# Performance work log

Hardware: AMD Instinct MI355X
Metric: run time of the kernel (lower is better)

## Reference

```python
import jax, jax.numpy as jnp
import numpy as np
from jax import lax

N, H, W = 8, 512, 512
INF = 1.0e6  # sentinel distance; INF**2 = 1e12 fits fp32


def _edt(feature):
    """Exact Euclidean distance transform. feature: (N,H,W) bool, True = zero-distance pixels.
    Separable: 1D column-distance per row via two scans, then min over rows of (di^2 + g^2).
    (cv2 DIST_L2 mask=3 is a chamfer approximation of this exact EDT.)"""
    g = jnp.where(feature, 0.0, INF)  # (N,H,W)
    cols = jnp.moveaxis(g, 2, 0)  # (W,N,H)

    def step(c, x):
        d = jnp.minimum(x, c + 1.0)
        return d, d

    init = jnp.full(g.shape[:2], INF, g.dtype)
    _, f = lax.scan(step, init, cols)
    _, b = lax.scan(step, init, f, reverse=True)
    g1 = jnp.moveaxis(b, 0, 2)  # (N,H,W) 1D distance along W
    g2 = g1 * g1
    rows = jnp.arange(g.shape[1], dtype=g.dtype)

    def per_row(i):
        # min over source rows k of (i-k)^2 + g2[:,k,:] -> (N,W)
        return jnp.min(g2 + ((i - rows) ** 2)[None, :, None], axis=1)

    d2 = lax.map(per_row, rows)  # (H,N,W)
    return jnp.sqrt(jnp.moveaxis(d2, 0, 1))  # (N,H,W)


def _signed_distance(gt):
    # gt: (N,1,H,W). Positive inside mask, negative outside; per-image normalized, clipped to [-1,1].
    m = gt[:, 0] > 0.5
    dist_in = _edt(~m)   # cv2.distanceTransform(m): distance to nearest zero pixel
    dist_out = _edt(m)   # cv2.distanceTransform(1-m)
    sd = dist_in - dist_out
    mx = jnp.max(sd, axis=(1, 2), keepdims=True)
    sd = jnp.where(mx > 0, sd / (mx + 1e-6), sd)
    return jnp.clip(sd, -1.0, 1.0)[:, None]  # (N,1,H,W)


def _bce(p, t):
    eps = 1e-7  # stand-in for torch BCELoss log clamp at -100
    p = jnp.clip(p, eps, 1.0 - eps)
    return -(t * jnp.log(p) + (1.0 - t) * jnp.log1p(-p))


def _loss(seg_pred, seg_gt, edge_pred, edge_gt,
          cb_edge=0.9, lam_dice=0.5, w_edge=0.5, w_boundary=0.2):
    # seg = BCE + lam_dice * Dice
    seg_bce = jnp.mean(_bce(seg_pred, seg_gt))
    inter = jnp.sum(seg_pred * seg_gt, axis=(2, 3))
    denom = jnp.sum(seg_pred, axis=(2, 3)) + jnp.sum(seg_gt, axis=(2, 3)) + 1e-6
    dice = 1.0 - jnp.mean(2.0 * inter / denom)
    seg = seg_bce + lam_dice * dice
    # edge = class-balanced BCE
    el = _bce(edge_pred, edge_gt)
    w = jnp.where(edge_gt > 0.5, cb_edge, 1.0 - cb_edge)
    edg = jnp.mean(el * w) * w_edge
    # boundary = |pred-gt| * |signed distance of gt| (sd is detached in the original)
    sd = lax.stop_gradient(_signed_distance(seg_gt))
    bdl = w_boundary * jnp.mean(jnp.abs(seg_pred - seg_gt) * jnp.abs(sd))
    return seg + edg + bdl


def setup_inputs() -> dict:
    key = jax.random.key(0)
    k1, k2, k3, k4 = jax.random.split(key, 4)
    shp = (N, 1, H, W)
    return {
        "seg_pred": jax.random.uniform(k1, shp, dtype=jnp.float32),
        "seg_gt": (jax.random.uniform(k2, shp) > 0.5).astype(jnp.float32),
        "edge_pred": jax.random.uniform(k3, shp, dtype=jnp.float32),
        "edge_gt": (jax.random.uniform(k4, shp) > 0.5).astype(jnp.float32),
    }


def reference(seg_pred, seg_gt, edge_pred, edge_gt):
    return _loss(seg_pred, seg_gt, edge_pred, edge_gt)
```

## Files before the change

### kernel.cpp

```cpp
#include <hip/hip_runtime.h>
#include <math.h>

#define HN 8
#define HH 512
#define HW 512
#define NPIX (HH*HW)
#define NTOT (HN*NPIX)
#define INF1D 1.0e6f
#define BIGF 3.0e38f
#define SQINF 4.4e9f

__global__ __launch_bounds__(256) void k_rows(const float* __restrict__ gt,
                                              unsigned int* __restrict__ packed) {
  const int lane = threadIdx.x & 63;
  const int wv   = threadIdx.x >> 6;
  const int row  = blockIdx.x * 4 + wv;
  const float* g = gt + (size_t)row * HW;

  float4 a0 = *(const float4*)(g + lane * 8);
  float4 a1 = *(const float4*)(g + lane * 8 + 4);
  float mv[8] = {a0.x, a0.y, a0.z, a0.w, a1.x, a1.y, a1.z, a1.w};

  float pin[8], pout[8], sfin[8], sfout[8];
  float rin = BIGF, rout = BIGF;
  for (int j = 0; j < 8; ++j) {
    float wf = (float)(lane * 8 + j);
    bool m = mv[j] > 0.5f;
    float gin  = m ? INF1D : 0.f;
    float gout = m ? 0.f : INF1D;
    rin  = fminf(rin,  gin  - wf);  pin[j]  = rin;
    rout = fminf(rout, gout - wf);  pout[j] = rout;
  }
  float xin = rin, xout = rout;
  for (int off = 1; off < 64; off <<= 1) {
    float yi = __shfl_up(xin, off);
    float yo = __shfl_up(xout, off);
    if (lane >= off) { xin = fminf(xin, yi); xout = fminf(xout, yo); }
  }
  float ein  = __shfl_up(xin, 1);  if (lane == 0) ein  = BIGF;
  float eout = __shfl_up(xout, 1); if (lane == 0) eout = BIGF;

  float rsin = BIGF, rsout = BIGF;
  for (int j = 7; j >= 0; --j) {
    float wf = (float)(lane * 8 + j);
    bool m = mv[j] > 0.5f;
    float gin  = m ? INF1D : 0.f;
    float gout = m ? 0.f : INF1D;
    rsin  = fminf(rsin,  gin  + wf);  sfin[j]  = rsin;
    rsout = fminf(rsout, gout + wf);  sfout[j] = rsout;
  }
  float zin = rsin, zout = rsout;
  for (int off = 1; off < 64; off <<= 1) {
    float yi = __shfl_down(zin, off);
    float yo = __shfl_down(zout, off);
    if (lane + off < 64) { zin = fminf(zin, yi); zout = fminf(zout, yo); }
  }
  float sein  = __shfl_down(zin, 1);  if (lane == 63) sein  = BIGF;
  float seout = __shfl_down(zout, 1); if (lane == 63) seout = BIGF;

  unsigned int outp[8];
  for (int j = 0; j < 8; ++j) {
    float wf = (float)(lane * 8 + j);
    float fin  = wf + fminf(pin[j],  ein);
    float fout = wf + fminf(pout[j], eout);
    float bin  = fminf(sfin[j],  sein)  - wf;
    float bout = fminf(sfout[j], seout) - wf;
    float g1i = fminf(fin,  bin);
    float g1o = fminf(fout, bout);
    unsigned int di = (g1i > 65534.f) ? 0xFFFFu : (unsigned int)(g1i + 0.5f);
    unsigned int dq = (g1o > 65534.f) ? 0xFFFFu : (unsigned int)(g1o + 0.5f);
    outp[j] = di | (dq << 16);
  }
  unsigned int* dst = packed + (size_t)row * HW + lane * 8;
  *(uint4*)dst       = make_uint4(outp[0], outp[1], outp[2], outp[3]);
  *(uint4*)(dst + 4) = make_uint4(outp[4], outp[5], outp[6], outp[7]);
}

#define ICH 64
#define HALO 32
__global__ __launch_bounds__(256) void k_cols(const unsigned int* __restrict__ packed,
                                              float* __restrict__ sd,
                                              float* __restrict__ partials) {
  __shared__ float sq[128 * 65];
  const int tid = threadIdx.x;
  const int wx = blockIdx.x;
  const int iy = blockIdx.y;
  const int n  = blockIdx.z;
  const int I0 = iy * ICH;
  const int kb = max(0, I0 - HALO);
  const int ke = min(HH, I0 + ICH + HALO);
  const int sz = ke - kb;
  const int w0 = wx * 64;
  const unsigned int* src = packed + (size_t)n * NPIX + (size_t)kb * HW + w0;

  const int total4 = sz * 16;
  for (int p4 = tid; p4 < total4; p4 += 256) {
    int row = p4 >> 4;
    int c4  = (p4 & 15) << 2;
    uint4 v = *(const uint4*)(src + (size_t)row * HW + c4);
    unsigned int u[4] = {v.x, v.y, v.z, v.w};
#pragma unroll
    for (int e = 0; e < 4; ++e) {
      unsigned int lo = u[e] & 0xFFFFu;
      unsigned int hi = u[e] >> 16;
      unsigned int d  = lo | hi;
      float dsq = (float)(d * d);
      sq[row * 65 + c4 + e] = (hi == 0u) ? dsq : -dsq;
    }
  }
  __syncthreads();

  const int lane = tid & 63;
  const int wv   = tid >> 6;
  const int col  = lane;
  const int base = (I0 - kb) + wv * 16;
  float lmax = -BIGF;

  for (int q = 0; q < 16; ++q) {
    const int li = base + q;
    const float own = sq[li * 65 + col];
    const bool  m   = own > 0.f;
    const float sgn = m ? 1.f : -1.f;
    float best = fabsf(own);
#pragma unroll
    for (int dk = 1; dk <= 8; ++dk) {
      const float dkk = (float)(dk * dk);
      int k1 = li - dk, k2 = li + dk;
      float a = sgn * sq[max(k1, 0) * 65 + col];
      float b = sgn * sq[min(k2, sz - 1) * 65 + col];
      float ta = (k1 >= 0) ? fmaxf(a, 0.f) : SQINF;
      float tb = (k2 < sz) ? fmaxf(b, 0.f) : SQINF;
      best = fminf(best, ta + dkk);
      best = fminf(best, tb + dkk);
    }
    for (int dk = 9; dk < 128; ++dk) {
      float dkk = (float)(dk * dk);
      if (__all(dkk >= best)) break;
      int k1 = li - dk, k2 = li + dk;
      float a = sgn * sq[max(k1, 0) * 65 + col];
      float b = sgn * sq[min(k2, sz - 1) * 65 + col];
      float ta = (k1 >= 0) ? fmaxf(a, 0.f) : SQINF;
      float tb = (k2 < sz) ? fmaxf(b, 0.f) : SQINF;
      best = fminf(best, ta + dkk);
      best = fminf(best, tb + dkk);
    }
    const int i = I0 + wv * 16 + q;
    float s = m ? sqrtf(best) : -sqrtf(best);
    sd[(size_t)n * NPIX + (size_t)i * HW + w0 + col] = s;
    lmax = fmaxf(lmax, s);
  }
  for (int off = 32; off; off >>= 1) lmax = fmaxf(lmax, __shfl_xor(lmax, off));
  if (lane == 0) partials[((n * 8 + iy) * 8 + wx) * 4 + wv] = lmax;
}

__global__ __launch_bounds__(256) void k_loss(const float* __restrict__ seg_p,
                                              const float* __restrict__ seg_t,
                                              const float* __restrict__ edge_p,
                                              const float* __restrict__ edge_t,
                                              const float* __restrict__ sd,
                                              const float* __restrict__ partials,
                                              float* __restrict__ partials2) {
  const int n = blockIdx.x >> 7;
  const int tid = threadIdx.x;
  const int wv = tid >> 6, ln = tid & 63;

  float v = partials[n * 256 + tid];
  for (int off = 32; off; off >>= 1) v = fmaxf(v, __shfl_xor(v, off));
  __shared__ float smax[4];
  if (ln == 0) smax[wv] = v;
  __syncthreads();
  const float mx = fmaxf(fmaxf(smax[0], smax[1]), fmaxf(smax[2], smax[3]));
  const float inv = (mx > 0.f) ? 1.f / (mx + 1e-6f) : 1.f;
  const float HI = 1.0f - 1e-7f;

  const size_t base = (size_t)n * NPIX + (size_t)(blockIdx.x & 127) * 2048
                    + (size_t)tid * 8;

  float a_bce = 0.f, a_pt = 0.f, a_ps = 0.f, a_ts = 0.f, a_ed = 0.f, a_bd = 0.f;
  for (int h = 0; h < 8; h += 4) {
    float4 p4  = *(const float4*)(seg_p  + base + h);
    float4 t4  = *(const float4*)(seg_t  + base + h);
    float4 ep4 = *(const float4*)(edge_p + base + h);
    float4 et4 = *(const float4*)(edge_t + base + h);
    float4 s4  = *(const float4*)(sd     + base + h);
    float pa[4]  = {p4.x, p4.y, p4.z, p4.w};
    float ta[4]  = {t4.x, t4.y, t4.z, t4.w};
    float epa[4] = {ep4.x, ep4.y, ep4.z, ep4.w};
    float eta[4] = {et4.x, et4.y, et4.z, et4.w};
    float sa[4]  = {s4.x, s4.y, s4.z, s4.w};
#pragma unroll
    for (int j = 0; j < 4; ++j) {
      float p = pa[j], t = ta[j];
      float pc = fminf(fmaxf(p, 1e-7f), HI);
      bool tm = t > 0.5f;
      a_bce -= __logf(tm ? pc : 1.f - pc);
      a_pt  += p * t;
      a_ps  += p;
      a_ts  += t;
      float ep = epa[j], et = eta[j];
      float ec = fminf(fmaxf(ep, 1e-7f), HI);
      bool em = et > 0.5f;
      a_ed -= __logf(em ? ec : 1.f - ec) * (em ? 0.9f : 0.1f);
      float sn = sa[j] * inv;
      sn = fminf(fmaxf(sn, -1.f), 1.f);
      a_bd += fabsf(p - t) * fabsf(sn);
    }
  }
  for (int off = 32; off; off >>= 1) {
    a_bce += __shfl_xor(a_bce, off);
    a_pt  += __shfl_xor(a_pt,  off);
    a_ps  += __shfl_xor(a_ps,  off);
    a_ts  += __shfl_xor(a_ts,  off);
    a_ed  += __shfl_xor(a_ed,  off);
    a_bd  += __shfl_xor(a_bd,  off);
  }
  __shared__ float red[4][6];
  if (ln == 0) {
    red[wv][0] = a_bce; red[wv][1] = a_pt; red[wv][2] = a_ps;
    red[wv][3] = a_ts;  red[wv][4] = a_ed; red[wv][5] = a_bd;
  }
  __syncthreads();
  if (tid == 0) {
    float* dst = partials2 + (size_t)blockIdx.x * 8;
    dst[0] = red[0][0] + red[1][0] + red[2][0] + red[3][0];
    dst[1] = red[0][1] + red[1][1] + red[2][1] + red[3][1];
    dst[2] = red[0][2] + red[1][2] + red[2][2] + red[3][2];
    dst[3] = red[0][3] + red[1][3] + red[2][3] + red[3][3];
    dst[4] = red[0][4] + red[1][4] + red[2][4] + red[3][4];
    dst[5] = red[0][5] + red[1][5] + red[2][5] + red[3][5];
  }
}

__global__ __launch_bounds__(256) void k_final(const float* __restrict__ partials2,
                                               float* __restrict__ out) {
  const int t = threadIdx.x;
  const int n = t >> 5;
  const int l = t & 31;
  float s0 = 0.f, s1 = 0.f, s2 = 0.f, s3 = 0.f, s4 = 0.f, s5 = 0.f;
#pragma unroll
  for (int it = 0; it < 4; ++it) {
    const float* p = partials2 + (size_t)((n * 128) + l + it * 32) * 8;
    s0 += p[0]; s1 += p[1]; s2 += p[2];
    s3 += p[3]; s4 += p[4]; s5 += p[5];
  }
  for (int off = 16; off; off >>= 1) {
    s0 += __shfl_xor(s0, off); s1 += __shfl_xor(s1, off);
    s2 += __shfl_xor(s2, off); s3 += __shfl_xor(s3, off);
    s4 += __shfl_xor(s4, off); s5 += __shfl_xor(s5, off);
  }
  __shared__ float red[8][6];
  if (l == 0) {
    red[n][0] = s0; red[n][1] = s1; red[n][2] = s2;
    red[n][3] = s3; red[n][4] = s4; red[n][5] = s5;
  }
  __syncthreads();
  if (t == 0) {
    const float M = (float)NTOT;
    float bce = 0.f, ed = 0.f, bd = 0.f, dsum = 0.f;
    for (int nn = 0; nn < HN; ++nn) {
      bce += red[nn][0]; ed += red[nn][4]; bd += red[nn][5];
      float den = red[nn][2] + red[nn][3] + 1e-6f;
      dsum += 2.f * red[nn][1] / den;
    }
    float dice = 1.f - dsum / (float)HN;
    out[0] = bce / M + 0.5f * dice + 0.5f * (ed / M) + 0.2f * (bd / M);
  }
}

extern "C" void kernel_launch(void* const* d_in, const int* in_sizes, int n_in,
                              void* d_out, int out_size, void* d_ws, size_t ws_size,
                              hipStream_t stream) {
  const float* seg_p  = (const float*)d_in[0];
  const float* seg_t  = (const float*)d_in[1];
  const float* edge_p = (const float*)d_in[2];
  const float* edge_t = (const float*)d_in[3];
  float* out = (float*)d_out;

  char* ws = (char*)d_ws;
  unsigned int* packed = (unsigned int*)ws;
  float* sd        = (float*)(ws + (size_t)NTOT * 4);
  float* partials  = (float*)(ws + (size_t)NTOT * 8);
  float* partials2 = partials + 8 * 256;

  k_rows<<<dim3(HN * HH / 4), 256, 0, stream>>>(seg_t, packed);
  k_cols<<<dim3(8, 8, HN), 256, 0, stream>>>(packed, sd, partials);
  k_loss<<<dim3(HN * 128), 256, 0, stream>>>(seg_p, seg_t, edge_p, edge_t, sd, partials, partials2);
  k_final<<<1, 256, 0, stream>>>(partials2, out);
}
```

Before: 103.3 us.

## Keep a sliding register window of column values in the EDT column kernel

The column pass now preloads a 17-row register window per thread and rotates it across the 16 output rows, so the first eight neighbour offsets come from registers instead of LDS reads. The LDS tile stride changes to 68 so the staging stores can be float4 vector writes. Boundary handling now clamps indices instead of substituting a large sentinel, which removes compares and selects but relies on clamped rows never producing a smaller minimum. The added window raises register pressure, which could lower occupancy.

```diff
diff --git a/kernel.cpp b/kernel.cpp
--- a/kernel.cpp
+++ b/kernel.cpp
@@ -8,7 +8,6 @@
 #define NTOT (HN*NPIX)
 #define INF1D 1.0e6f
 #define BIGF 3.0e38f
-#define SQINF 4.4e9f
 
 __global__ __launch_bounds__(256) void k_rows(const float* __restrict__ gt,
                                               unsigned int* __restrict__ packed) {
@@ -78,10 +77,11 @@
 
 #define ICH 64
 #define HALO 32
+#define LSTR 68
 __global__ __launch_bounds__(256) void k_cols(const unsigned int* __restrict__ packed,
                                               float* __restrict__ sd,
                                               float* __restrict__ partials) {
-  __shared__ float sq[128 * 65];
+  __shared__ float sq[128 * LSTR];
   const int tid = threadIdx.x;
   const int wx = blockIdx.x;
   const int iy = blockIdx.y;
@@ -99,14 +99,16 @@
     int c4  = (p4 & 15) << 2;
     uint4 v = *(const uint4*)(src + (size_t)row * HW + c4);
     unsigned int u[4] = {v.x, v.y, v.z, v.w};
+    float f[4];
 #pragma unroll
     for (int e = 0; e < 4; ++e) {
       unsigned int lo = u[e] & 0xFFFFu;
       unsigned int hi = u[e] >> 16;
       unsigned int d  = lo | hi;
       float dsq = (float)(d * d);
-      sq[row * 65 + c4 + e] = (hi == 0u) ? dsq : -dsq;
-    }
+      f[e] = (hi == 0u) ? dsq : -dsq;
+    }
+    *(float4*)&sq[row * LSTR + c4] = make_float4(f[0], f[1], f[2], f[3]);
   }
   __syncthreads();
 
@@ -116,38 +118,44 @@
   const int base = (I0 - kb) + wv * 16;
   float lmax = -BIGF;
 
+  float w[17];
+#pragma unroll
+  for (int t = 0; t < 17; ++t) {
+    int rw = min(max(base - 8 + t, 0), sz - 1);
+    w[t] = sq[rw * LSTR + col];
+  }
+
+#pragma unroll
   for (int q = 0; q < 16; ++q) {
-    const int li = base + q;
-    const float own = sq[li * 65 + col];
+    const float own = w[(8 + q) % 17];
     const bool  m   = own > 0.f;
     const float sgn = m ? 1.f : -1.f;
     float best = fabsf(own);
 #pragma unroll
     for (int dk = 1; dk <= 8; ++dk) {
       const float dkk = (float)(dk * dk);
-      int k1 = li - dk, k2 = li + dk;
-      float a = sgn * sq[max(k1, 0) * 65 + col];
-      float b = sgn * sq[min(k2, sz - 1) * 65 + col];
-      float ta = (k1 >= 0) ? fmaxf(a, 0.f) : SQINF;
-      float tb = (k2 < sz) ? fmaxf(b, 0.f) : SQINF;
-      best = fminf(best, ta + dkk);
-      best = fminf(best, tb + dkk);
-    }
+      float a = fmaxf(sgn * w[(8 + q - dk + 17) % 17], 0.f);
+      float b = fmaxf(sgn * w[(8 + q + dk) % 17],      0.f);
+      best = fminf(best, a + dkk);
+      best = fminf(best, b + dkk);
+    }
+    const int li = base + q;
     for (int dk = 9; dk < 128; ++dk) {
       float dkk = (float)(dk * dk);
       if (__all(dkk >= best)) break;
-      int k1 = li - dk, k2 = li + dk;
-      float a = sgn * sq[max(k1, 0) * 65 + col];
-      float b = sgn * sq[min(k2, sz - 1) * 65 + col];
-      float ta = (k1 >= 0) ? fmaxf(a, 0.f) : SQINF;
-      float tb = (k2 < sz) ? fmaxf(b, 0.f) : SQINF;
-      best = fminf(best, ta + dkk);
-      best = fminf(best, tb + dkk);
+      float a = fmaxf(sgn * sq[max(li - dk, 0) * LSTR + col], 0.f);
+      float b = fmaxf(sgn * sq[min(li + dk, sz - 1) * LSTR + col], 0.f);
+      best = fminf(best, a + dkk);
+      best = fminf(best, b + dkk);
     }
     const int i = I0 + wv * 16 + q;
     float s = m ? sqrtf(best) : -sqrtf(best);
     sd[(size_t)n * NPIX + (size_t)i * HW + w0 + col] = s;
     lmax = fmaxf(lmax, s);
+    if (q < 15) {
+      int rw = min(base + q + 9, sz - 1);
+      w[q % 17] = sq[rw * LSTR + col];
+    }
   }
   for (int off = 32; off; off >>= 1) lmax = fmaxf(lmax, __shfl_xor(lmax, off));
   if (lane == 0) partials[((n * 8 + iy) * 8 + wx) * 4 + wv] = lmax;
```

Measured after the change: 97.62 us. 1.06x faster.
